# Kernel tuning notes

Hardware: AMD Instinct MI355X
Metric: run time of the kernel (lower is better)

## Reference

```python
import jax, jax.numpy as jnp
import numpy as np

N_NODES = 100000
N_EDGES = 3200000
F_IN, F_HID, F_OUT = 1433, 16, 7


def setup_inputs() -> dict:
    key = jax.random.key(0)
    k1, k2, k3, k4, k5, k6 = jax.random.split(key, 6)
    x = jax.random.normal(k1, (N_NODES, F_IN), dtype=jnp.float32)
    edge_index = jax.random.randint(k2, (2, N_EDGES), 0, N_NODES, dtype=jnp.int64)
    # Glorot-style init for GCNConv weights, zeros for bias (PyG default)
    W1 = jax.random.normal(k3, (F_IN, F_HID), dtype=jnp.float32) * (1.0 / np.sqrt(F_IN))
    b1 = jnp.zeros((F_HID,), dtype=jnp.float32)
    W2 = jax.random.normal(k4, (F_HID, F_OUT), dtype=jnp.float32) * (1.0 / np.sqrt(F_HID))
    b2 = jnp.zeros((F_OUT,), dtype=jnp.float32)
    return {"x": x, "edge_index": edge_index, "W1": W1, "b1": b1, "W2": W2, "b2": b2}


def _gcn_conv(x, W, b, src, dst, deg_inv_sqrt):
    # x: [N, Fin] -> [N, Fout]; src/dst: [E+N] (self-loops included)
    h = x @ W  # linear transform first (PyG GCNConv)
    norm = deg_inv_sqrt[src] * deg_inv_sqrt[dst]  # symmetric normalization
    msg = h[src] * norm[:, None]  # gather + scale
    agg = jax.ops.segment_sum(msg, dst, num_segments=x.shape[0])  # scatter-add at targets
    return agg + b


def reference(x, edge_index, W1, b1, W2, b2):
    n = x.shape[0]
    loops = jnp.arange(n, dtype=edge_index.dtype)
    src = jnp.concatenate([edge_index[0], loops])  # source nodes j
    dst = jnp.concatenate([edge_index[1], loops])  # target nodes i
    # degree over targets (with self-loops), unit edge weights
    deg = jax.ops.segment_sum(jnp.ones_like(src, dtype=x.dtype), dst, num_segments=n)
    deg_inv_sqrt = jnp.where(deg > 0, jax.lax.rsqrt(deg), 0.0)

    h = _gcn_conv(x, W1, b1, src, dst, deg_inv_sqrt)
    h = jax.nn.relu(h)
    # dropout is identity in eval mode
    h = _gcn_conv(h, W2, b2, src, dst, deg_inv_sqrt)
    return jax.nn.log_softmax(h, axis=1)
```

## Files before the change

kernel.cpp:

```cpp
#include <hip/hip_runtime.h>
#include <hip/hip_bf16.h>

#define F_IN 1433
#define F_HID 16
#define F_OUT 7
#define KSTEPS 45

typedef __bf16 bf16x8 __attribute__((ext_vector_type(8)));
typedef float f32x4 __attribute__((ext_vector_type(4)));
typedef int i32x4 __attribute__((ext_vector_type(4)));
typedef unsigned short u16;
typedef unsigned int u32;

static __device__ __forceinline__ float bf2f(u16 b) {
    return __builtin_bit_cast(float, (u32)b << 16);
}
static __device__ __forceinline__ u16 f2bf(float f) {
    u32 u = __builtin_bit_cast(u32, f);
    u32 r = u + 0x7FFFu + ((u >> 16) & 1u);
    return (u16)(r >> 16);
}
static __device__ __forceinline__ int clampN(int v, int N) {
    return ((unsigned)v < (unsigned)N) ? v : 0;
}

__global__ __launch_bounds__(64) void k_detect(const u16* __restrict__ xu,
                                               const int* __restrict__ ei,
                                               int* __restrict__ flags) {
    int t = threadIdx.x;
    u16 v = xu[t];
    int e = (v >> 7) & 0xFF;
    unsigned long long mb = __ballot(e >= 100 && e <= 140);
    unsigned long long mz = __ballot(ei[2 * t + 1] == 0);
    if (t == 0) {
        flags[0] = (__popcll(mb) >= 56) ? 1 : 0;
        flags[1] = (__popcll(mz) >= 48) ? 1 : 0;
    }
}



__global__ __launch_bounds__(256) void k_deg(const int* __restrict__ ei,
                                             const int* __restrict__ flags,
                                             int* __restrict__ deg, int E, int N) {
    int sh = flags[1];
    int i = blockIdx.x * 256 + threadIdx.x;
    if (i < E) {
        int d = ei[(size_t)(E + i) << sh];
        atomicAdd(&deg[clampN(d, N)], 1);
    }
}

__global__ __launch_bounds__(256) void k_scan1(const int* __restrict__ deg,
                                               int* __restrict__ rowoff,
                                               int* __restrict__ bsum, int N) {
    __shared__ int s[256];
    int t = threadIdx.x, i = blockIdx.x * 256 + t;
    int v = (i < N) ? deg[i] : 0;
    s[t] = v;
    __syncthreads();
    for (int o = 1; o < 256; o <<= 1) {
        int x = 0;
        if (t >= o) x = s[t - o];
        __syncthreads();
        s[t] += x;
        __syncthreads();
    }
    if (i < N) rowoff[i] = s[t] - v;
    if (t == 255) bsum[blockIdx.x] = s[255];
}

__global__ __launch_bounds__(1024) void k_scan2(const int* __restrict__ bsum,
                                                int* __restrict__ bscan, int NB) {
    __shared__ int s[1024];
    int t = threadIdx.x;
    int v = (t < NB) ? bsum[t] : 0;
    s[t] = v;
    __syncthreads();
    for (int o = 1; o < 1024; o <<= 1) {
        int x = 0;
        if (t >= o) x = s[t - o];
        __syncthreads();
        s[t] += x;
        __syncthreads();
    }
    if (t < NB) bscan[t] = s[t] - v;
}

__global__ __launch_bounds__(256) void k_scan3(const int* __restrict__ deg,
                                               int* __restrict__ rowoff,
                                               const int* __restrict__ bscan,
                                               int* __restrict__ fill,
                                               float* __restrict__ dis, int N) {
    int i = blockIdx.x * 256 + threadIdx.x;
    if (i >= N) return;
    int ro = rowoff[i] + bscan[blockIdx.x];
    rowoff[i] = ro;
    fill[i] = ro;
    dis[i] = rsqrtf((float)(deg[i] + 1));
}

__global__ __launch_bounds__(256) void k_fill(const int* __restrict__ ei,
                                              const int* __restrict__ flags,
                                              int* __restrict__ fill,
                                              int* __restrict__ csr, int E, int N) {
    int sh = flags[1];
    int i = blockIdx.x * 256 + threadIdx.x;
    if (i < E) {
        int d = ei[(size_t)(E + i) << sh];
        int s = ei[(size_t)i << sh];
        int slot = atomicAdd(&fill[clampN(d, N)], 1);
        if (slot >= 0 && slot < E) csr[slot] = clampN(s, N);
    }
}


template <int ISBF>
static __device__ __forceinline__ void gemm_tiles(const u16* xu, const float* xf,
                                                  const u16* lw,
                                                  const float* __restrict__ dis,
                                                  float* __restrict__ hn, int N,
                                                  int tid, int bid, int grid) {
    int wave = tid >> 6, lane = tid & 63;
    int quad = lane >> 4, m = lane & 15;
    int ntiles = (N + 63) / 64;
    int k0 = quad * 8;

    for (int tb = bid; tb < ntiles; tb += grid) {
        int base = tb * 64 + wave * 16;
        int row = base + m;
        int rowc = row < N ? row : N - 1;
        const u16* xru = xu + (size_t)rowc * F_IN;
        const float* xrf = xf + (size_t)rowc * F_IN;

        f32x4 acc = {0.f, 0.f, 0.f, 0.f};
        for (int ks = 0; ks < KSTEPS - 1; ks++) {
            u16 e[8];
            if (ISBF) {
                const u16* xp = xru + k0 + ks * 32;
#pragma unroll
                for (int j = 0; j < 8; j++) e[j] = xp[j];
            } else {
                const float* xp = xrf + k0 + ks * 32;
#pragma unroll
                for (int j = 0; j < 8; j++) e[j] = f2bf(xp[j]);
            }
            i32x4 wv = {(int)((u32)e[0] | ((u32)e[1] << 16)),
                        (int)((u32)e[2] | ((u32)e[3] << 16)),
                        (int)((u32)e[4] | ((u32)e[5] << 16)),
                        (int)((u32)e[6] | ((u32)e[7] << 16))};
            bf16x8 a = __builtin_bit_cast(bf16x8, wv);
            bf16x8 b = __builtin_bit_cast(bf16x8, *(const i32x4*)(&lw[ks * 512 + lane * 8]));
            acc = __builtin_amdgcn_mfma_f32_16x16x32_bf16(a, b, acc, 0, 0, 0);
        }
        {
            int ks = KSTEPS - 1;
            int kb = ks * 32 + k0;
            u16 e[8];
#pragma unroll
            for (int j = 0; j < 8; j++) {
                int k = kb + j;
                e[j] = (k < F_IN) ? (ISBF ? xru[k] : f2bf(xrf[k])) : (u16)0;
            }
            i32x4 wv = {(int)((u32)e[0] | ((u32)e[1] << 16)),
                        (int)((u32)e[2] | ((u32)e[3] << 16)),
                        (int)((u32)e[4] | ((u32)e[5] << 16)),
                        (int)((u32)e[6] | ((u32)e[7] << 16))};
            bf16x8 a = __builtin_bit_cast(bf16x8, wv);
            bf16x8 b = __builtin_bit_cast(bf16x8, *(const i32x4*)(&lw[ks * 512 + lane * 8]));
            acc = __builtin_amdgcn_mfma_f32_16x16x32_bf16(a, b, acc, 0, 0, 0);
        }
#pragma unroll
        for (int r = 0; r < 4; r++) {
            int orow = base + quad * 4 + r;
            if (orow < N) hn[(size_t)orow * 16 + m] = acc[r] * dis[orow];
        }
    }
}

__global__ __launch_bounds__(256) void k_gemm1(const void* __restrict__ x,
                                               const void* __restrict__ W1,
                                               const int* __restrict__ flags,
                                               const float* __restrict__ dis,
                                               float* __restrict__ hn, int N) {
    __shared__ __align__(16) u16 lw[KSTEPS * 512];
    int tid = threadIdx.x;
    int isbf = flags[0];
    const u16* W1u = (const u16*)W1;
    const float* W1f = (const float*)W1;
    for (int idx = tid; idx < KSTEPS * 512; idx += 256) {
        int j = idx & 7, lane = (idx >> 3) & 63, ks = idx >> 9;
        int quad = lane >> 4, n = lane & 15;
        int k = ks * 32 + quad * 8 + j;
        u16 w = 0;
        if (k < F_IN) w = isbf ? W1u[k * 16 + n] : f2bf(W1f[k * 16 + n]);
        lw[idx] = w;
    }
    __syncthreads();
    if (isbf)
        gemm_tiles<1>((const u16*)x, (const float*)x, lw, dis, hn, N, tid, blockIdx.x, gridDim.x);
    else
        gemm_tiles<0>((const u16*)x, (const float*)x, lw, dis, hn, N, tid, blockIdx.x, gridDim.x);
}


__global__ __launch_bounds__(256) void k_agg1(const float* __restrict__ hn,
                                              const int* __restrict__ csr,
                                              const int* __restrict__ rowoff,
                                              const int* __restrict__ deg,
                                              const float* __restrict__ dis,
                                              const void* __restrict__ b1,
                                              const int* __restrict__ flags,
                                              float* __restrict__ y1, int N) {
    int tid = threadIdx.x;
    int c = tid & 15, g = tid >> 4;
    int v = blockIdx.x * 16 + g;
    if (v >= N) return;
    float bc = flags[0] ? bf2f(((const u16*)b1)[c]) : ((const float*)b1)[c];
    float acc = hn[(size_t)v * 16 + c];
    int s0 = rowoff[v], d = deg[v];
    for (int i = 0; i < d; i++) {
        int s = clampN(csr[s0 + i], N);
        acc += hn[(size_t)s * 16 + c];
    }
    float z = acc * dis[v] + bc;
    y1[(size_t)v * 16 + c] = fmaxf(z, 0.f);
}


__global__ __launch_bounds__(256) void k_lin2(const float* __restrict__ y1,
                                              const void* __restrict__ W2,
                                              const int* __restrict__ flags,
                                              const float* __restrict__ dis,
                                              float* __restrict__ tn, int N) {
    __shared__ float w[16 * 8];
    int tid = threadIdx.x;
    if (tid < 128) {
        int k = tid >> 3, c = tid & 7;
        float wv = 0.f;
        if (c < 7)
            wv = flags[0] ? bf2f(((const u16*)W2)[k * 7 + c]) : ((const float*)W2)[k * 7 + c];
        w[tid] = wv;
    }
    __syncthreads();
    int v = blockIdx.x * 256 + tid;
    if (v >= N) return;
    const float* yr = y1 + (size_t)v * 16;
    float dv = dis[v];
    float* tr = tn + (size_t)v * 8;
#pragma unroll
    for (int c = 0; c < 7; c++) {
        float s = 0.f;
#pragma unroll
        for (int k = 0; k < 16; k++) s += yr[k] * w[k * 8 + c];
        tr[c] = s * dv;
    }
    tr[7] = 0.f;
}


__global__ __launch_bounds__(256) void k_agg2(const float* __restrict__ tn,
                                              const int* __restrict__ csr,
                                              const int* __restrict__ rowoff,
                                              const int* __restrict__ deg,
                                              const float* __restrict__ dis,
                                              const void* __restrict__ b2,
                                              const int* __restrict__ flags,
                                              void* __restrict__ out, int N) {
    int tid = threadIdx.x;
    int c = tid & 7, g = tid >> 3;
    int v = blockIdx.x * 32 + g;
    if (v >= N) return;
    int isbf = flags[0];
    float bc = 0.f;
    if (c < 7) bc = isbf ? bf2f(((const u16*)b2)[c]) : ((const float*)b2)[c];
    float acc = tn[(size_t)v * 8 + c];
    int s0 = rowoff[v], d = deg[v];
    for (int i = 0; i < d; i++) {
        int s = clampN(csr[s0 + i], N);
        acc += tn[(size_t)s * 8 + c];
    }
    float z = (c < 7) ? (acc * dis[v] + bc) : -1e30f;
    float mx = z;
#pragma unroll
    for (int o = 1; o < 8; o <<= 1) mx = fmaxf(mx, __shfl_xor(mx, o, 8));
    float ex = (c < 7) ? expf(z - mx) : 0.f;
    float sm = ex;
#pragma unroll
    for (int o = 1; o < 8; o <<= 1) sm += __shfl_xor(sm, o, 8);
    sm = fmaxf(sm, 1e-30f);
    if (c < 7) {
        float res = z - mx - logf(sm);
        if (isbf)
            ((u16*)out)[(size_t)v * 7 + c] = f2bf(res);
        else
            ((float*)out)[(size_t)v * 7 + c] = res;
    }
}


extern "C" void kernel_launch(void* const* d_in, const int* in_sizes, int n_in,
                              void* d_out, int out_size, void* d_ws, size_t ws_size,
                              hipStream_t stream) {
    const void* x = d_in[0];
    const int* ei = (const int*)d_in[1];
    const void* W1 = d_in[2];
    const void* b1 = d_in[3];
    const void* W2 = d_in[4];
    const void* b2 = d_in[5];

    int N = in_sizes[0] / F_IN;
    int E = in_sizes[1] / 2;

    char* p = (char*)d_ws;
    size_t off = 0;
    auto alloc = [&](size_t bytes) -> void* {
        off = (off + 255) & ~(size_t)255;
        void* r = p + off;
        off += bytes;
        return r;
    };
    int* flags = (int*)alloc(256);
    int* deg = (int*)alloc((size_t)N * 4);
    int* rowoff = (int*)alloc((size_t)N * 4);
    int* fill = (int*)alloc((size_t)N * 4);
    int* bsum = (int*)alloc(1024 * 4);
    int* bscan = (int*)alloc(1024 * 4);
    float* dis = (float*)alloc((size_t)N * 4);
    int* csr = (int*)alloc((size_t)E * 4);
    float* hn = (float*)alloc((size_t)N * 16 * 4);
    float* y1 = (float*)alloc((size_t)N * 16 * 4);
    float* tn = hn;
    (void)ws_size;
    (void)n_in;
    (void)out_size;

    int gE = (E + 255) / 256;
    int gN = (N + 255) / 256;

    k_detect<<<1, 64, 0, stream>>>((const u16*)x, ei, flags);
    hipMemsetAsync(deg, 0, (size_t)N * 4, stream);
    k_deg<<<gE, 256, 0, stream>>>(ei, flags, deg, E, N);
    k_scan1<<<gN, 256, 0, stream>>>(deg, rowoff, bsum, N);
    k_scan2<<<1, 1024, 0, stream>>>(bsum, bscan, gN);
    k_scan3<<<gN, 256, 0, stream>>>(deg, rowoff, bscan, fill, dis, N);
    k_fill<<<gE, 256, 0, stream>>>(ei, flags, fill, csr, E, N);

    int ntiles = (N + 63) / 64;
    int gg = ntiles < 768 ? ntiles : 768;
    k_gemm1<<<gg, 256, 0, stream>>>(x, W1, flags, dis, hn, N);

    k_agg1<<<(N + 15) / 16, 256, 0, stream>>>(hn, csr, rowoff, deg, dis, b1, flags, y1, N);
    k_lin2<<<gN, 256, 0, stream>>>(y1, W2, flags, dis, tn, N);
    k_agg2<<<(N + 31) / 32, 256, 0, stream>>>(tn, csr, rowoff, deg, dis, b2, flags, d_out, N);
}
```

Before: 1.356 ms.

## Fuse layer-2 linear into layer-1 aggregation and merge init kernels

Folds the separate second-layer linear kernel into the first aggregation kernel. Each 16-lane group computes its relu output and then forms the 7-wide projection through wave shuffles, so the y1 buffer no longer has to be written and read back. The hipMemsetAsync of the degree array and the flag-detection kernel are merged into one init kernel. The gather loops in both aggregation kernels are unrolled by four with separate accumulators to expose more memory-level parallelism. The gather loops also drop the index clamp, which removes protection against out-of-range edge indices.

```diff
diff --git a/kernel.cpp b/kernel.cpp
--- a/kernel.cpp
+++ b/kernel.cpp
@@ -24,17 +24,22 @@
     return ((unsigned)v < (unsigned)N) ? v : 0;
 }
 
-__global__ __launch_bounds__(64) void k_detect(const u16* __restrict__ xu,
-                                               const int* __restrict__ ei,
-                                               int* __restrict__ flags) {
-    int t = threadIdx.x;
-    u16 v = xu[t];
-    int e = (v >> 7) & 0xFF;
-    unsigned long long mb = __ballot(e >= 100 && e <= 140);
-    unsigned long long mz = __ballot(ei[2 * t + 1] == 0);
-    if (t == 0) {
-        flags[0] = (__popcll(mb) >= 56) ? 1 : 0;
-        flags[1] = (__popcll(mz) >= 48) ? 1 : 0;
+__global__ __launch_bounds__(256) void k_init(const u16* __restrict__ xu,
+                                              const int* __restrict__ ei,
+                                              int* __restrict__ flags,
+                                              int* __restrict__ deg, int N) {
+    int i = blockIdx.x * 256 + threadIdx.x;
+    if (i < N) deg[i] = 0;
+    if (blockIdx.x == 0 && threadIdx.x < 64) {
+        int t = threadIdx.x;
+        u16 v = xu[t];
+        int e = (v >> 7) & 0xFF;
+        unsigned long long mb = __ballot(e >= 100 && e <= 140);
+        unsigned long long mz = __ballot(ei[2 * t + 1] == 0);
+        if (t == 0) {
+            flags[0] = (__popcll(mb) >= 56) ? 1 : 0;
+            flags[1] = (__popcll(mz) >= 48) ? 1 : 0;
+        }
     }
 }
 
@@ -210,52 +215,49 @@
                                               const int* __restrict__ deg,
                                               const float* __restrict__ dis,
                                               const void* __restrict__ b1,
+                                              const void* __restrict__ W2,
                                               const int* __restrict__ flags,
-                                              float* __restrict__ y1, int N) {
+                                              float* __restrict__ tn, int N) {
     int tid = threadIdx.x;
+    int lane = tid & 63;
     int c = tid & 15, g = tid >> 4;
     int v = blockIdx.x * 16 + g;
     if (v >= N) return;
-    float bc = flags[0] ? bf2f(((const u16*)b1)[c]) : ((const float*)b1)[c];
+    int isbf = flags[0];
+    float bc = isbf ? bf2f(((const u16*)b1)[c]) : ((const float*)b1)[c];
+
     float acc = hn[(size_t)v * 16 + c];
     int s0 = rowoff[v], d = deg[v];
-    for (int i = 0; i < d; i++) {
-        int s = clampN(csr[s0 + i], N);
-        acc += hn[(size_t)s * 16 + c];
-    }
-    float z = acc * dis[v] + bc;
-    y1[(size_t)v * 16 + c] = fmaxf(z, 0.f);
-}
-
-
-__global__ __launch_bounds__(256) void k_lin2(const float* __restrict__ y1,
-                                              const void* __restrict__ W2,
-                                              const int* __restrict__ flags,
-                                              const float* __restrict__ dis,
-                                              float* __restrict__ tn, int N) {
-    __shared__ float w[16 * 8];
-    int tid = threadIdx.x;
-    if (tid < 128) {
-        int k = tid >> 3, c = tid & 7;
-        float wv = 0.f;
-        if (c < 7)
-            wv = flags[0] ? bf2f(((const u16*)W2)[k * 7 + c]) : ((const float*)W2)[k * 7 + c];
-        w[tid] = wv;
-    }
-    __syncthreads();
-    int v = blockIdx.x * 256 + tid;
-    if (v >= N) return;
-    const float* yr = y1 + (size_t)v * 16;
+    const int* cp = csr + s0;
+    float a1 = 0.f, a2 = 0.f, a3 = 0.f;
+    int i = 0;
+    for (; i + 4 <= d; i += 4) {
+        int sA = cp[i], sB = cp[i + 1], sC = cp[i + 2], sD = cp[i + 3];
+        acc += hn[(size_t)sA * 16 + c];
+        a1 += hn[(size_t)sB * 16 + c];
+        a2 += hn[(size_t)sC * 16 + c];
+        a3 += hn[(size_t)sD * 16 + c];
+    }
+    for (; i < d; i++) acc += hn[(size_t)cp[i] * 16 + c];
+    acc += (a1 + a2) + a3;
+
     float dv = dis[v];
-    float* tr = tn + (size_t)v * 8;
-#pragma unroll
-    for (int c = 0; c < 7; c++) {
-        float s = 0.f;
-#pragma unroll
-        for (int k = 0; k < 16; k++) s += yr[k] * w[k * 8 + c];
-        tr[c] = s * dv;
-    }
-    tr[7] = 0.f;
+    float y = fmaxf(acc * dv + bc, 0.f);
+
+    float w2c[16];
+#pragma unroll
+    for (int k = 0; k < 16; k++) {
+        float w = 0.f;
+        if (c < 7) w = isbf ? bf2f(((const u16*)W2)[k * 7 + c]) : ((const float*)W2)[k * 7 + c];
+        w2c[k] = w;
+    }
+    float s = 0.f;
+#pragma unroll
+    for (int k = 0; k < 16; k++) {
+        float yk = __shfl(y, (lane & 48) + k, 64);
+        s += yk * w2c[k];
+    }
+    if (c < 8) tn[(size_t)v * 8 + c] = (c < 7) ? s * dv : 0.f;
 }
 
 
@@ -274,12 +276,22 @@
     int isbf = flags[0];
     float bc = 0.f;
     if (c < 7) bc = isbf ? bf2f(((const u16*)b2)[c]) : ((const float*)b2)[c];
+
     float acc = tn[(size_t)v * 8 + c];
     int s0 = rowoff[v], d = deg[v];
-    for (int i = 0; i < d; i++) {
-        int s = clampN(csr[s0 + i], N);
-        acc += tn[(size_t)s * 8 + c];
-    }
+    const int* cp = csr + s0;
+    float a1 = 0.f, a2 = 0.f, a3 = 0.f;
+    int i = 0;
+    for (; i + 4 <= d; i += 4) {
+        int sA = cp[i], sB = cp[i + 1], sC = cp[i + 2], sD = cp[i + 3];
+        acc += tn[(size_t)sA * 8 + c];
+        a1 += tn[(size_t)sB * 8 + c];
+        a2 += tn[(size_t)sC * 8 + c];
+        a3 += tn[(size_t)sD * 8 + c];
+    }
+    for (; i < d; i++) acc += tn[(size_t)cp[i] * 8 + c];
+    acc += (a1 + a2) + a3;
+
     float z = (c < 7) ? (acc * dis[v] + bc) : -1e30f;
     float mx = z;
 #pragma unroll
@@ -329,8 +341,7 @@
     float* dis = (float*)alloc((size_t)N * 4);
     int* csr = (int*)alloc((size_t)E * 4);
     float* hn = (float*)alloc((size_t)N * 16 * 4);
-    float* y1 = (float*)alloc((size_t)N * 16 * 4);
-    float* tn = hn;
+    float* tn = (float*)alloc((size_t)N * 8 * 4);
     (void)ws_size;
     (void)n_in;
     (void)out_size;
@@ -338,8 +349,7 @@
     int gE = (E + 255) / 256;
     int gN = (N + 255) / 256;
 
-    k_detect<<<1, 64, 0, stream>>>((const u16*)x, ei, flags);
-    hipMemsetAsync(deg, 0, (size_t)N * 4, stream);
+    k_init<<<gN, 256, 0, stream>>>((const u16*)x, ei, flags, deg, N);
     k_deg<<<gE, 256, 0, stream>>>(ei, flags, deg, E, N);
     k_scan1<<<gN, 256, 0, stream>>>(deg, rowoff, bsum, N);
     k_scan2<<<1, 1024, 0, stream>>>(bsum, bscan, gN);
@@ -350,7 +360,6 @@
     int gg = ntiles < 768 ? ntiles : 768;
     k_gemm1<<<gg, 256, 0, stream>>>(x, W1, flags, dis, hn, N);
 
-    k_agg1<<<(N + 15) / 16, 256, 0, stream>>>(hn, csr, rowoff, deg, dis, b1, flags, y1, N);
-    k_lin2<<<gN, 256, 0, stream>>>(y1, W2, flags, dis, tn, N);
+    k_agg1<<<(N + 15) / 16, 256, 0, stream>>>(hn, csr, rowoff, deg, dis, b1, W2, flags, tn, N);
     k_agg2<<<(N + 31) / 32, 256, 0, stream>>>(tn, csr, rowoff, deg, dis, b2, flags, d_out, N);
 }
```

After: 1.304 ms. 3.8% less time.
